# Kernel tuning notes

Hardware: AMD Instinct MI355X
Metric: run time of the kernel (lower is better)

The kernel has to match this reference:

```python
import jax, jax.numpy as jnp
import numpy as np

NUM_GRAPHS = 8
NEG_SLOPE = 0.2


def add_self_loops(edge_index, n):
    loops = jnp.arange(n, dtype=edge_index.dtype)
    src = jnp.concatenate([edge_index[0], loops])
    dst = jnp.concatenate([edge_index[1], loops])
    return src, dst


def gat_conv(x, src, dst, W, att_src, att_dst, bias, concat):
    # x: [N, F_in]; W: [F_in, H*C]; att_src/att_dst: [H, C]; bias: [H*C] or [C]
    n = x.shape[0]
    H, C = att_src.shape
    xl = (x @ W).reshape(n, H, C)                     # [N, H, C]
    a_src = jnp.einsum('nhc,hc->nh', xl, att_src)     # [N, H]
    a_dst = jnp.einsum('nhc,hc->nh', xl, att_dst)     # [N, H]
    e = jax.nn.leaky_relu(a_src[src] + a_dst[dst], NEG_SLOPE)  # [E, H]
    # segment softmax over edges grouped by destination node
    m = jax.ops.segment_max(e, dst, num_segments=n)   # [N, H]
    e = jnp.exp(e - m[dst])
    denom = jax.ops.segment_sum(e, dst, num_segments=n)
    alpha = e / (denom[dst] + 1e-16)                  # [E, H]
    msg = xl[src] * alpha[:, :, None]                 # [E, H, C]
    out = jax.ops.segment_sum(msg, dst, num_segments=n)  # [N, H, C]
    out = out.reshape(n, H * C) if concat else out.mean(axis=1)
    return out + bias


def global_mean_pool(x, batch, num_graphs):
    s = jax.ops.segment_sum(x, batch, num_segments=num_graphs)
    cnt = jax.ops.segment_sum(jnp.ones((x.shape[0],), x.dtype), batch, num_segments=num_graphs)
    return s / jnp.maximum(cnt, 1.0)[:, None]


def setup_inputs() -> dict:
    key = jax.random.key(0)
    ks = jax.random.split(key, 12)
    N, E, F_in, Ch, H, F_out = 50000, 800000, 128, 64, 4, 128
    x = jax.random.normal(ks[0], (N, F_in), dtype=jnp.float32)
    edge_index = jax.random.randint(ks[1], (2, E), 0, N, dtype=jnp.int64)
    batch = jnp.sort(jax.random.randint(ks[2], (N,), 0, NUM_GRAPHS, dtype=jnp.int64))
    s = 0.1
    W1 = jax.random.normal(ks[3], (F_in, H * Ch), dtype=jnp.float32) * s
    att_src1 = jax.random.normal(ks[4], (H, Ch), dtype=jnp.float32) * s
    att_dst1 = jax.random.normal(ks[5], (H, Ch), dtype=jnp.float32) * s
    bias1 = jnp.zeros((H * Ch,), dtype=jnp.float32)
    W2 = jax.random.normal(ks[6], (H * Ch, F_out), dtype=jnp.float32) * s
    att_src2 = jax.random.normal(ks[7], (1, F_out), dtype=jnp.float32) * s
    att_dst2 = jax.random.normal(ks[8], (1, F_out), dtype=jnp.float32) * s
    bias2 = jnp.zeros((F_out,), dtype=jnp.float32)
    return {"x": x, "edge_index": edge_index, "batch": batch,
            "W1": W1, "att_src1": att_src1, "att_dst1": att_dst1, "bias1": bias1,
            "W2": W2, "att_src2": att_src2, "att_dst2": att_dst2, "bias2": bias2}


def reference(x, edge_index, batch, W1, att_src1, att_dst1, bias1, W2, att_src2, att_dst2, bias2):
    n = x.shape[0]
    src, dst = add_self_loops(edge_index, n)
    h = gat_conv(x, src, dst, W1, att_src1, att_dst1, bias1, concat=True)
    h = jax.nn.relu(h)
    h = gat_conv(h, src, dst, W2, att_src2, att_dst2, bias2, concat=False)
    return global_mean_pool(h, batch, NUM_GRAPHS)
```

## Files before the change

kernel.cpp:

```cpp
#include <hip/hip_runtime.h>
#include <cstdint>
#include <cstddef>

#define NEG_SLOPE 0.2f
#define LOG2E 1.44269504088896f
#define NREP 64

typedef __attribute__((ext_vector_type(8))) short bf16x8;
typedef __attribute__((ext_vector_type(4))) float f32x4;
typedef __attribute__((ext_vector_type(2))) float f32x2;

__device__ __forceinline__ ushort f2b(float f) {
  unsigned u = __float_as_uint(f);
  return (ushort)((u + 0x7FFFu + ((u >> 16) & 1)) >> 16);
}
__device__ __forceinline__ float fexp2(float x) {
#if __has_builtin(__builtin_amdgcn_exp2f)
  return __builtin_amdgcn_exp2f(x);
#else
  return __exp2f(x);
#endif
}
__device__ __forceinline__ int lbound(const int* __restrict__ a, int n, int key) {
  int lo = 0, hi = n;
  while (lo < hi) { int m = (lo + hi) >> 1; if (a[m] < key) lo = m + 1; else hi = m; }
  return lo;
}

__global__ __launch_bounds__(256) void setup_k(const float* __restrict__ W1,
                                               ushort* __restrict__ Bp1,
                                               const float* __restrict__ W2,
                                               ushort* __restrict__ Bp2,
                                               int* __restrict__ hist,
                                               float* __restrict__ pp, int n) {
  int i = blockIdx.x * 256 + threadIdx.x;
  {
    int k = i >> 8, c = i & 255;
    Bp1[(((size_t)(k >> 3) * 256 + c) << 3) + (k & 7)] = f2b(W1[i]);
  }
  {
    int k = i >> 7, c = i & 127;
    Bp2[(((size_t)(k >> 3) * 128 + c) << 3) + (k & 7)] = f2b(W2[i]);
  }
  if (i < n) hist[i] = 0;
  int i2 = i + 32768;
  if (i2 < n) hist[i2] = 0;
  pp[i] = 0.f;
  pp[i + 32768] = 0.f;
}

template<int N, int K, int C, int H, bool AF32>
__device__ __forceinline__ void gemm_attn_body(const void* __restrict__ A_,
                                               const ushort* __restrict__ Bp,
                                               const float* __restrict__ att_src,
                                               const float* __restrict__ att_dst,
                                               unsigned char* __restrict__ C8,
                                               float* __restrict__ a_src,
                                               float* __restrict__ a_dst,
                                               int M, int bid) {
  constexpr int ROWS = K / 8;
  __shared__ ushort Bl[ROWS * N * 8];
  const int tid = threadIdx.x;
  #pragma unroll
  for (int it = 0; it < ROWS * N / 256; ++it) {
    int id = it * 256 + tid;
    int brow = id / N, c = id % N;
    int cs = (c + 2 * brow) & (N - 1);
    *(bf16x8*)&Bl[((size_t)brow * N + cs) * 8] = *(const bf16x8*)&Bp[(size_t)id * 8];
  }
  __syncthreads();

  const int wave = tid >> 6;
  const int lane = tid & 63;
  const int strips = M / 16;
  const int strip = bid * 4 + wave;
  if (strip >= strips) return;
  const int r = lane & 15, kg = lane >> 4;
  const int nrow = strip * 16 + r;

  bf16x8 a[K / 32];
  if constexpr (AF32) {
    const float* Af = (const float*)A_;
    #pragma unroll
    for (int k0 = 0; k0 < K / 32; ++k0) {
      float4 f0 = *(const float4*)(Af + (size_t)nrow * K + k0 * 32 + kg * 8);
      float4 f1 = *(const float4*)(Af + (size_t)nrow * K + k0 * 32 + kg * 8 + 4);
      bf16x8 t;
      t[0] = (short)f2b(f0.x); t[1] = (short)f2b(f0.y);
      t[2] = (short)f2b(f0.z); t[3] = (short)f2b(f0.w);
      t[4] = (short)f2b(f1.x); t[5] = (short)f2b(f1.y);
      t[6] = (short)f2b(f1.z); t[7] = (short)f2b(f1.w);
      a[k0] = t;
    }
  } else {
    const ushort* Ab = (const ushort*)A_;
    #pragma unroll
    for (int k0 = 0; k0 < K / 32; ++k0)
      a[k0] = *(const bf16x8*)(Ab + (size_t)nrow * K + k0 * 32 + kg * 8);
  }

  float as_p = 0.f, ad_p = 0.f;
  #pragma unroll
  for (int n0 = 0; n0 < N / 16; ++n0) {
    f32x4 acc = {0.f, 0.f, 0.f, 0.f};
    #pragma unroll
    for (int k0 = 0; k0 < K / 32; ++k0) {
      int brow = k0 * 4 + kg;
      int cs = (n0 * 16 + r + 2 * brow) & (N - 1);
      bf16x8 b = *(const bf16x8*)&Bl[((size_t)brow * N + cs) * 8];
      acc = __builtin_amdgcn_mfma_f32_16x16x32_bf16(b, a[k0], acc, 0, 0, 0);
    }
    float4 avs = *(const float4*)(att_src + n0 * 16 + kg * 4);
    float4 avd = *(const float4*)(att_dst + n0 * 16 + kg * 4);
    as_p += acc[0] * avs.x + acc[1] * avs.y + acc[2] * avs.z + acc[3] * avs.w;
    ad_p += acc[0] * avd.x + acc[1] * avd.y + acc[2] * avd.z + acc[3] * avd.w;
    int dw = __builtin_amdgcn_cvt_pk_fp8_f32(acc[0], acc[1], 0, false);
    dw = __builtin_amdgcn_cvt_pk_fp8_f32(acc[2], acc[3], dw, true);
    *(unsigned*)(C8 + (size_t)nrow * N + (uint)(n0 * 16 + kg * 4)) = (unsigned)dw;
    if (((n0 + 1) * 16) % C == 0) {
      float ts = as_p * LOG2E, td = ad_p * LOG2E;
      ts += __shfl_xor(ts, 16); ts += __shfl_xor(ts, 32);
      td += __shfl_xor(td, 16); td += __shfl_xor(td, 32);
      if (kg == 0) {
        int h = (n0 * 16) / C;
        a_src[(size_t)nrow * H + h] = ts;
        a_dst[(size_t)nrow * H + h] = td;
      }
      as_p = 0.f; ad_p = 0.f;
    }
  }
}

template<int N, int K, int C, int H, bool AF32>
__global__ __launch_bounds__(256) void gemm_rank_k(const void* __restrict__ A_,
                                                   const ushort* __restrict__ Bp,
                                                   const float* __restrict__ att_src,
                                                   const float* __restrict__ att_dst,
                                                   unsigned char* __restrict__ C8,
                                                   float* __restrict__ a_src,
                                                   float* __restrict__ a_dst, int M,
                                                   const int* __restrict__ edst,
                                                   int* __restrict__ hist,
                                                   int* __restrict__ rank,
                                                   int E, int GB) {
  if ((int)blockIdx.x < GB) {
    gemm_attn_body<N, K, C, H, AF32>(A_, Bp, att_src, att_dst, C8,
                                     a_src, a_dst, M, blockIdx.x);
  } else {
    int base = ((blockIdx.x - GB) * 256 + threadIdx.x) * 8;
    #pragma unroll
    for (int u = 0; u < 8; ++u) {
      int e = base + u;
      if (e < E) rank[e] = atomicAdd(hist + edst[e], 1);
    }
  }
}

template<int N, int K, int C, int H, bool AF32>
__global__ __launch_bounds__(256) void gemm_attn_k(const void* __restrict__ A_,
                                                   const ushort* __restrict__ Bp,
                                                   const float* __restrict__ att_src,
                                                   const float* __restrict__ att_dst,
                                                   unsigned char* __restrict__ C8,
                                                   float* __restrict__ a_src,
                                                   float* __restrict__ a_dst, int M) {
  gemm_attn_body<N, K, C, H, AF32>(A_, Bp, att_src, att_dst, C8,
                                   a_src, a_dst, M, blockIdx.x);
}

__global__ __launch_bounds__(256) void scan1_k(const int* __restrict__ hist,
                                               int* __restrict__ excl,
                                               int* __restrict__ chunksum, int n) {
  __shared__ int sums[256];
  int base = blockIdx.x * 1024 + threadIdx.x * 4;
  int4 v = {0, 0, 0, 0};
  if (base + 3 < n) v = *(const int4*)(hist + base);
  else {
    if (base < n)     v.x = hist[base];
    if (base + 1 < n) v.y = hist[base + 1];
    if (base + 2 < n) v.z = hist[base + 2];
    if (base + 3 < n) v.w = hist[base + 3];
  }
  int s = v.x + v.y + v.z + v.w;
  sums[threadIdx.x] = s;
  __syncthreads();
  for (int off = 1; off < 256; off <<= 1) {
    int t = (threadIdx.x >= (unsigned)off) ? sums[threadIdx.x - off] : 0;
    __syncthreads();
    sums[threadIdx.x] += t;
    __syncthreads();
  }
  if (threadIdx.x == 255) chunksum[blockIdx.x] = sums[255];
  int e0 = sums[threadIdx.x] - s;
  int e1 = e0 + v.x, e2 = e1 + v.y, e3 = e2 + v.z;
  if (base + 3 < n) {
    int4 o = {e0, e1, e2, e3};
    *(int4*)(excl + base) = o;
  } else {
    if (base < n)     excl[base] = e0;
    if (base + 1 < n) excl[base + 1] = e1;
    if (base + 2 < n) excl[base + 2] = e2;
    if (base + 3 < n) excl[base + 3] = e3;
  }
}

__global__ void scan2_k(const int* __restrict__ chunksum,
                        int* __restrict__ chunkoff, int nchunks) {
  if (threadIdx.x == 0) {
    int run = 0;
    for (int c = 0; c < nchunks; ++c) { chunkoff[c] = run; run += chunksum[c]; }
  }
}

__global__ __launch_bounds__(256) void addoff_k(int* __restrict__ rowptr,
                                                const int* __restrict__ chunkoff,
                                                int n, int total) {
  int i = blockIdx.x * 256 + threadIdx.x;
  if (i == 0) rowptr[n] = total;
  if (i >= n) return;
  rowptr[i] += chunkoff[i >> 10];
}

__global__ __launch_bounds__(256) void fill_k(const int* __restrict__ esrc,
                                              const int* __restrict__ edst,
                                              const int* __restrict__ rowptr,
                                              const int* __restrict__ rank,
                                              int* __restrict__ csr_src,
                                              int E, int Epad) {
  int e = blockIdx.x * 256 + threadIdx.x;
  if (e < E) csr_src[rowptr[edst[e]] + rank[e]] = esrc[e];
  else if (e < Epad) csr_src[e] = 0;
}

template<int H, int C>
__global__ __launch_bounds__(256) void agg1_k(const int* __restrict__ rowptr,
                                              const int* __restrict__ csr,
                                              const float* __restrict__ a_src,
                                              const float* __restrict__ a_dst,
                                              const unsigned char* __restrict__ xl,
                                              const float* __restrict__ bias,
                                              ushort* __restrict__ out, int n) {
  constexpr int F = H * C;
  const int wid0 = (blockIdx.x * 256 + threadIdx.x) >> 6;
  if (wid0 >= n) return;
  const int wid = __builtin_amdgcn_readfirstlane(wid0);
  const int lane = threadIdx.x & 63;
  const int h = lane >> 4;
  const uint lofs = (uint)lane * 4;
  const int j4 = lane & 3;
  const int je = lane >> 2;
  const int beg = rowptr[wid];
  const int end = rowptr[wid + 1];

  const float adh_s = a_dst[(uint)wid * 4 + j4];
  float vs_s = a_src[(uint)wid * 4 + j4] + adh_s;
  vs_s = fmaxf(vs_s, NEG_SLOPE * vs_s);

  float den = 1.f;
  float acc[4];
  {
    uint xs = *(const uint*)(xl + ((uint)wid * F + lofs));
    f32x2 lo = __builtin_amdgcn_cvt_pk_f32_fp8(xs, false);
    f32x2 hi = __builtin_amdgcn_cvt_pk_f32_fp8(xs, true);
    acc[0] = lo[0]; acc[1] = lo[1]; acc[2] = hi[0]; acc[3] = hi[1];
  }

  for (int j = beg; j < end; j += 16) {
    int sl = csr[j + je];
    float t = a_src[(uint)sl * 4 + j4] + adh_s;
    t = fmaxf(t, NEG_SLOPE * t);
    t = (j + je < end) ? t - vs_s : -1e30f;
    float pl = fexp2(t);
    uint xv[16];
    #pragma unroll
    for (int u = 0; u < 16; ++u) {
      int su = csr[j + u];
      xv[u] = *(const uint*)(xl + ((uint)su * F + lofs));
    }
    #pragma unroll
    for (int u = 0; u < 16; ++u) {
      float pu = __shfl(pl, u * 4 + h);
      den += pu;
      f32x2 lo = __builtin_amdgcn_cvt_pk_f32_fp8(xv[u], false);
      f32x2 hi = __builtin_amdgcn_cvt_pk_f32_fp8(xv[u], true);
      acc[0] = fmaf(pu, lo[0], acc[0]);
      acc[1] = fmaf(pu, lo[1], acc[1]);
      acc[2] = fmaf(pu, hi[0], acc[2]);
      acc[3] = fmaf(pu, hi[1], acc[3]);
    }
  }

  float inv = 1.f / (den + 1e-16f);
  float o[4];
  #pragma unroll
  for (int i = 0; i < 4; ++i)
    o[i] = fmaxf(fmaf(acc[i], inv, bias[lane * 4 + i]), 0.f);
  ushort4 ov = {f2b(o[0]), f2b(o[1]), f2b(o[2]), f2b(o[3])};
  *(ushort4*)(out + (size_t)wid * F + lane * 4) = ov;
}

__global__ __launch_bounds__(256) void agg2pool_k(const int* __restrict__ rowptr,
                                                  const int* __restrict__ csr,
                                                  const float* __restrict__ a_src,
                                                  const float* __restrict__ a_dst,
                                                  const unsigned char* __restrict__ xl,
                                                  const int* __restrict__ batch,
                                                  float* __restrict__ pp,
                                                  int n, int Emax) {
  const int pair = (blockIdx.x * 256 + threadIdx.x) >> 6;
  const int lane = threadIdx.x & 63;
  const int l32 = lane & 31;
  const int half = lane >> 5;
  int wid = pair * 2 + half;
  const bool act = wid < n;
  if (!act) wid = n - 1;
  const uint lofs = (uint)l32 * 4;
  const int beg = rowptr[wid];
  const int deg = rowptr[wid + 1] - beg;
  const int mdeg = max(deg, __shfl_xor(deg, 32));
  const float adh = a_dst[wid];

  float vs = a_src[wid] + adh;
  vs = fmaxf(vs, NEG_SLOPE * vs);
  float den = 1.f;
  float acc[4];
  {
    uint xs = *(const uint*)(xl + ((uint)wid * 128 + lofs));
    f32x2 lo = __builtin_amdgcn_cvt_pk_f32_fp8(xs, false);
    f32x2 hi = __builtin_amdgcn_cvt_pk_f32_fp8(xs, true);
    acc[0] = lo[0]; acc[1] = lo[1]; acc[2] = hi[0]; acc[3] = hi[1];
  }

  for (int j = 0; j < mdeg; j += 32) {
    int sl = csr[min(beg + j + l32, Emax)];
    float t = a_src[sl] + adh;
    t = fmaxf(t, NEG_SLOPE * t);
    t = (j + l32 < deg) ? t - vs : -1e30f;
    float pl = fexp2(t);
    #pragma unroll
    for (int g = 0; g < 2; ++g) {
      int su[16];
      uint xv[16];
      #pragma unroll
      for (int u = 0; u < 16; ++u) {
        su[u] = __shfl(sl, half * 32 + g * 16 + u);
        xv[u] = *(const uint*)(xl + ((uint)su[u] * 128 + lofs));
      }
      #pragma unroll
      for (int u = 0; u < 16; ++u) {
        float pu = __shfl(pl, half * 32 + g * 16 + u);
        den += pu;
        f32x2 lo = __builtin_amdgcn_cvt_pk_f32_fp8(xv[u], false);
        f32x2 hi = __builtin_amdgcn_cvt_pk_f32_fp8(xv[u], true);
        acc[0] = fmaf(pu, lo[0], acc[0]);
        acc[1] = fmaf(pu, lo[1], acc[1]);
        acc[2] = fmaf(pu, hi[0], acc[2]);
        acc[3] = fmaf(pu, hi[1], acc[3]);
      }
    }
  }

  __shared__ float red[8][128];
  __shared__ int gids[8];
  const int rrow = (threadIdx.x >> 6) * 2 + half;
  float inv = act ? 1.f / (den + 1e-16f) : 0.f;
  float4 ov = {acc[0] * inv, acc[1] * inv, acc[2] * inv, acc[3] * inv};
  *(float4*)&red[rrow][l32 * 4] = ov;
  if (l32 == 0) gids[rrow] = act ? batch[wid] : -1;
  __syncthreads();
  if (threadIdx.x < 128) {
    const int ch = threadIdx.x;
    float* base = pp + (size_t)(blockIdx.x & (NREP - 1)) * 8 * 128;
    float sum = 0.f;
    int cur = gids[0];
    #pragma unroll
    for (int r = 0; r < 8; ++r) {
      int g = gids[r];
      if (g != cur) {
        if (cur >= 0) unsafeAtomicAdd(base + cur * 128 + ch, sum);
        sum = 0.f;
        cur = g;
      }
      if (g >= 0) sum += red[r][ch];
    }
    if (cur >= 0) unsafeAtomicAdd(base + cur * 128 + ch, sum);
  }
}

__global__ __launch_bounds__(256) void finalize_k(const float* __restrict__ pp,
                                                  const int* __restrict__ batch,
                                                  const float* __restrict__ bias2,
                                                  float* __restrict__ out, int n) {
  int t = blockIdx.x * 256 + threadIdx.x;
  if (t >= 8 * 128) return;
  int g = t >> 7, c = t & 127;
  float s = 0.f;
  #pragma unroll 8
  for (int rep = 0; rep < NREP; ++rep) s += pp[rep * 8 * 128 + t];
  int lo = lbound(batch, n, g);
  int hi = lbound(batch, n, g + 1);
  float cnt = (float)(hi - lo);
  out[t] = s / fmaxf(cnt, 1.f) + bias2[c];
}

extern "C" void kernel_launch(void* const* d_in, const int* in_sizes, int n_in,
                              void* d_out, int out_size, void* d_ws, size_t ws_size,
                              hipStream_t stream) {
  const float* x        = (const float*)d_in[0];
  const int*   ei       = (const int*)d_in[1];
  const int*   batch    = (const int*)d_in[2];
  const float* W1       = (const float*)d_in[3];
  const float* att_src1 = (const float*)d_in[4];
  const float* att_dst1 = (const float*)d_in[5];
  const float* bias1    = (const float*)d_in[6];
  const float* W2       = (const float*)d_in[7];
  const float* att_src2 = (const float*)d_in[8];
  const float* att_dst2 = (const float*)d_in[9];
  const float* bias2    = (const float*)d_in[10];
  float* out = (float*)d_out;

  const int E  = in_sizes[1] / 2;
  const int NN = in_sizes[2];
  const int* esrc = ei;
  const int* edst = ei + E;
  const int PAD = 64;

  char* w = (char*)d_ws;
  size_t woff = 0;
  auto walloc = [&](size_t bytes) -> char* {
    char* r = w + woff;
    woff += (bytes + 255) & ~(size_t)255;
    return r;
  };
  unsigned char* xl1 = (unsigned char*)walloc((size_t)NN * 256);
  ushort* h1     = (ushort*)walloc((size_t)NN * 256 * 2);
  unsigned char* xl2 = (unsigned char*)walloc((size_t)NN * 128);
  float*  a_src1 = (float*)walloc((size_t)NN * 4 * 4);
  float*  a_dst1 = (float*)walloc((size_t)NN * 4 * 4);
  float*  a_src2 = (float*)walloc((size_t)NN * 4);
  float*  a_dst2 = (float*)walloc((size_t)NN * 4);
  int*    rowptr = (int*)walloc((size_t)(NN + 1) * 4);
  int*    hist   = (int*)walloc((size_t)NN * 4);
  int*    rank   = (int*)walloc((size_t)E * 4);
  int*    csrsrc = (int*)walloc((size_t)(E + PAD) * 4);
  ushort* Bp1    = (ushort*)walloc(128 * 256 * 2);
  ushort* Bp2    = (ushort*)walloc(256 * 128 * 2);
  int*    chunks = (int*)walloc(256 * 4);
  int*    chunko = (int*)walloc(256 * 4);
  float*  pp     = (float*)walloc((size_t)NREP * 8 * 128 * 4);

  dim3 blk(256);
  const int nbEp = (E + PAD + 255) / 256;
  const int nbN4 = (NN + 3) / 4;
  const int nbP  = ((NN + 1) / 2 + 3) / 4;
  const int strips = NN / 16;
  const int gblocks = (strips + 3) / 4;
  const int rankBlocks = (E + 2047) / 2048;
  const int nchunks = (NN + 1023) / 1024;

  setup_k<<<128, blk, 0, stream>>>(W1, Bp1, W2, Bp2, hist, pp, NN);

  gemm_rank_k<256, 128, 64, 4, true><<<gblocks + rankBlocks, blk, 0, stream>>>(
      x, Bp1, att_src1, att_dst1, xl1, a_src1, a_dst1, NN,
      edst, hist, rank, E, gblocks);

  scan1_k<<<nchunks, blk, 0, stream>>>(hist, rowptr, chunks, NN);
  scan2_k<<<1, 64, 0, stream>>>(chunks, chunko, nchunks);
  addoff_k<<<(NN + 255) / 256, blk, 0, stream>>>(rowptr, chunko, NN, E);

  fill_k<<<nbEp, blk, 0, stream>>>(esrc, edst, rowptr, rank, csrsrc, E, E + PAD);

  agg1_k<4, 64><<<nbN4, blk, 0, stream>>>(
      rowptr, csrsrc, a_src1, a_dst1, xl1, bias1, h1, NN);

  gemm_attn_k<128, 256, 128, 1, false><<<gblocks, blk, 0, stream>>>(
      h1, Bp2, att_src2, att_dst2, xl2, a_src2, a_dst2, NN);

  agg2pool_k<<<nbP, blk, 0, stream>>>(
      rowptr, csrsrc, a_src2, a_dst2, xl2, batch, pp, NN, E + PAD - 1);

  finalize_k<<<4, blk, 0, stream>>>(pp, batch, bias2, out, NN);
}
```

Baseline: 164.4 us.

## Split rank and GEMM kernels, read B weights from global instead of LDS

Separates the fused GEMM+edge-rank kernel into a standalone rank kernel and a plain GEMM kernel. The GEMM no longer stages the packed bf16 weight matrix into swizzled shared memory and instead loads B fragments straight from global memory (L2-cached), with the n0 loop unroll reduced to 2. This removes the per-block LDS fill and barrier and lowers LDS use for occupancy. In exchange, every MFMA operand now comes from global memory, the rank atomics no longer overlap with the GEMM, and there is one extra kernel launch.

```diff
diff --git a/kernel.cpp b/kernel.cpp
--- a/kernel.cpp
+++ b/kernel.cpp
@@ -49,31 +49,29 @@
   pp[i + 32768] = 0.f;
 }
 
+__global__ __launch_bounds__(256) void rank_k(const int* __restrict__ edst,
+                                              int* __restrict__ hist,
+                                              int* __restrict__ rank, int E) {
+  int base = (blockIdx.x * 256 + threadIdx.x) * 8;
+  #pragma unroll
+  for (int u = 0; u < 8; ++u) {
+    int e = base + u;
+    if (e < E) rank[e] = atomicAdd(hist + edst[e], 1);
+  }
+}
+
 template<int N, int K, int C, int H, bool AF32>
-__device__ __forceinline__ void gemm_attn_body(const void* __restrict__ A_,
-                                               const ushort* __restrict__ Bp,
-                                               const float* __restrict__ att_src,
-                                               const float* __restrict__ att_dst,
-                                               unsigned char* __restrict__ C8,
-                                               float* __restrict__ a_src,
-                                               float* __restrict__ a_dst,
-                                               int M, int bid) {
-  constexpr int ROWS = K / 8;
-  __shared__ ushort Bl[ROWS * N * 8];
-  const int tid = threadIdx.x;
-  #pragma unroll
-  for (int it = 0; it < ROWS * N / 256; ++it) {
-    int id = it * 256 + tid;
-    int brow = id / N, c = id % N;
-    int cs = (c + 2 * brow) & (N - 1);
-    *(bf16x8*)&Bl[((size_t)brow * N + cs) * 8] = *(const bf16x8*)&Bp[(size_t)id * 8];
-  }
-  __syncthreads();
-
-  const int wave = tid >> 6;
-  const int lane = tid & 63;
+__global__ __launch_bounds__(256) void gemm_attn_k(const void* __restrict__ A_,
+                                                   const ushort* __restrict__ Bp,
+                                                   const float* __restrict__ att_src,
+                                                   const float* __restrict__ att_dst,
+                                                   unsigned char* __restrict__ C8,
+                                                   float* __restrict__ a_src,
+                                                   float* __restrict__ a_dst, int M) {
+  const int wave = threadIdx.x >> 6;
+  const int lane = threadIdx.x & 63;
   const int strips = M / 16;
-  const int strip = bid * 4 + wave;
+  const int strip = blockIdx.x * 4 + wave;
   if (strip >= strips) return;
   const int r = lane & 15, kg = lane >> 4;
   const int nrow = strip * 16 + r;
@@ -100,14 +98,12 @@
   }
 
   float as_p = 0.f, ad_p = 0.f;
-  #pragma unroll
+  #pragma unroll 2
   for (int n0 = 0; n0 < N / 16; ++n0) {
     f32x4 acc = {0.f, 0.f, 0.f, 0.f};
     #pragma unroll
     for (int k0 = 0; k0 < K / 32; ++k0) {
-      int brow = k0 * 4 + kg;
-      int cs = (n0 * 16 + r + 2 * brow) & (N - 1);
-      bf16x8 b = *(const bf16x8*)&Bl[((size_t)brow * N + cs) * 8];
+      bf16x8 b = *(const bf16x8*)(Bp + ((size_t)(k0 * 4 + kg) * N + n0 * 16 + r) * 8);
       acc = __builtin_amdgcn_mfma_f32_16x16x32_bf16(b, a[k0], acc, 0, 0, 0);
     }
     float4 avs = *(const float4*)(att_src + n0 * 16 + kg * 4);
@@ -129,43 +125,6 @@
       as_p = 0.f; ad_p = 0.f;
     }
   }
-}
-
-template<int N, int K, int C, int H, bool AF32>
-__global__ __launch_bounds__(256) void gemm_rank_k(const void* __restrict__ A_,
-                                                   const ushort* __restrict__ Bp,
-                                                   const float* __restrict__ att_src,
-                                                   const float* __restrict__ att_dst,
-                                                   unsigned char* __restrict__ C8,
-                                                   float* __restrict__ a_src,
-                                                   float* __restrict__ a_dst, int M,
-                                                   const int* __restrict__ edst,
-                                                   int* __restrict__ hist,
-                                                   int* __restrict__ rank,
-                                                   int E, int GB) {
-  if ((int)blockIdx.x < GB) {
-    gemm_attn_body<N, K, C, H, AF32>(A_, Bp, att_src, att_dst, C8,
-                                     a_src, a_dst, M, blockIdx.x);
-  } else {
-    int base = ((blockIdx.x - GB) * 256 + threadIdx.x) * 8;
-    #pragma unroll
-    for (int u = 0; u < 8; ++u) {
-      int e = base + u;
-      if (e < E) rank[e] = atomicAdd(hist + edst[e], 1);
-    }
-  }
-}
-
-template<int N, int K, int C, int H, bool AF32>
-__global__ __launch_bounds__(256) void gemm_attn_k(const void* __restrict__ A_,
-                                                   const ushort* __restrict__ Bp,
-                                                   const float* __restrict__ att_src,
-                                                   const float* __restrict__ att_dst,
-                                                   unsigned char* __restrict__ C8,
-                                                   float* __restrict__ a_src,
-                                                   float* __restrict__ a_dst, int M) {
-  gemm_attn_body<N, K, C, H, AF32>(A_, Bp, att_src, att_dst, C8,
-                                   a_src, a_dst, M, blockIdx.x);
 }
 
 __global__ __launch_bounds__(256) void scan1_k(const int* __restrict__ hist,
@@ -460,9 +419,10 @@
 
   setup_k<<<128, blk, 0, stream>>>(W1, Bp1, W2, Bp2, hist, pp, NN);
 
-  gemm_rank_k<256, 128, 64, 4, true><<<gblocks + rankBlocks, blk, 0, stream>>>(
-      x, Bp1, att_src1, att_dst1, xl1, a_src1, a_dst1, NN,
-      edst, hist, rank, E, gblocks);
+  rank_k<<<rankBlocks, blk, 0, stream>>>(edst, hist, rank, E);
+
+  gemm_attn_k<256, 128, 64, 4, true><<<gblocks, blk, 0, stream>>>(
+      x, Bp1, att_src1, att_dst1, xl1, a_src1, a_dst1, NN);
 
   scan1_k<<<nchunks, blk, 0, stream>>>(hist, rowptr, chunks, NN);
   scan2_k<<<1, 64, 0, stream>>>(chunks, chunko, nchunks);
```

After: 184.5 us. 12.3% more time.

## Split edge histogram into four replicas and read GEMM weights directly from global

Applied to the files above, without the earlier changes.

The destination-degree histogram is split into four sub-histograms indexed by edge id mod 4, which spreads atomic contention across replicas. The scan kernel now builds per-replica prefix offsets, and the CSR fill adds those offsets to compute each edge's slot. Separately, the GEMM no longer stages the packed weight matrix into LDS with a barrier; it loads B fragments straight from global/L2, and the n-loop unroll is reduced to 2. This removes the LDS staging and sync but adds more global loads per MFMA and extra memory traffic in the scan and fill kernels.

```diff
diff --git a/kernel.cpp b/kernel.cpp
--- a/kernel.cpp
+++ b/kernel.cpp
@@ -31,8 +31,8 @@
                                                ushort* __restrict__ Bp1,
                                                const float* __restrict__ W2,
                                                ushort* __restrict__ Bp2,
-                                               int* __restrict__ hist,
-                                               float* __restrict__ pp, int n) {
+                                               int* __restrict__ hist, int ns4,
+                                               float* __restrict__ pp) {
   int i = blockIdx.x * 256 + threadIdx.x;
   {
     int k = i >> 8, c = i & 255;
@@ -42,9 +42,7 @@
     int k = i >> 7, c = i & 127;
     Bp2[(((size_t)(k >> 3) * 128 + c) << 3) + (k & 7)] = f2b(W2[i]);
   }
-  if (i < n) hist[i] = 0;
-  int i2 = i + 32768;
-  if (i2 < n) hist[i2] = 0;
+  for (int j = i; j < ns4; j += 32768) hist[j] = 0;
   pp[i] = 0.f;
   pp[i + 32768] = 0.f;
 }
@@ -58,20 +56,8 @@
                                                float* __restrict__ a_src,
                                                float* __restrict__ a_dst,
                                                int M, int bid) {
-  constexpr int ROWS = K / 8;
-  __shared__ ushort Bl[ROWS * N * 8];
-  const int tid = threadIdx.x;
-  #pragma unroll
-  for (int it = 0; it < ROWS * N / 256; ++it) {
-    int id = it * 256 + tid;
-    int brow = id / N, c = id % N;
-    int cs = (c + 2 * brow) & (N - 1);
-    *(bf16x8*)&Bl[((size_t)brow * N + cs) * 8] = *(const bf16x8*)&Bp[(size_t)id * 8];
-  }
-  __syncthreads();
-
-  const int wave = tid >> 6;
-  const int lane = tid & 63;
+  const int wave = threadIdx.x >> 6;
+  const int lane = threadIdx.x & 63;
   const int strips = M / 16;
   const int strip = bid * 4 + wave;
   if (strip >= strips) return;
@@ -100,14 +86,12 @@
   }
 
   float as_p = 0.f, ad_p = 0.f;
-  #pragma unroll
+  #pragma unroll 2
   for (int n0 = 0; n0 < N / 16; ++n0) {
     f32x4 acc = {0.f, 0.f, 0.f, 0.f};
     #pragma unroll
     for (int k0 = 0; k0 < K / 32; ++k0) {
-      int brow = k0 * 4 + kg;
-      int cs = (n0 * 16 + r + 2 * brow) & (N - 1);
-      bf16x8 b = *(const bf16x8*)&Bl[((size_t)brow * N + cs) * 8];
+      bf16x8 b = *(const bf16x8*)(Bp + ((size_t)(k0 * 4 + kg) * N + n0 * 16 + r) * 8);
       acc = __builtin_amdgcn_mfma_f32_16x16x32_bf16(b, a[k0], acc, 0, 0, 0);
     }
     float4 avs = *(const float4*)(att_src + n0 * 16 + kg * 4);
@@ -140,7 +124,7 @@
                                                    float* __restrict__ a_src,
                                                    float* __restrict__ a_dst, int M,
                                                    const int* __restrict__ edst,
-                                                   int* __restrict__ hist,
+                                                   int* __restrict__ hist, int ns,
                                                    int* __restrict__ rank,
                                                    int E, int GB) {
   if ((int)blockIdx.x < GB) {
@@ -151,7 +135,8 @@
     #pragma unroll
     for (int u = 0; u < 8; ++u) {
       int e = base + u;
-      if (e < E) rank[e] = atomicAdd(hist + edst[e], 1);
+      if (e < E)
+        rank[e] = atomicAdd(hist + (e & 3) * ns + edst[e], 1);
     }
   }
 }
@@ -168,31 +153,47 @@
                                    a_src, a_dst, M, blockIdx.x);
 }
 
-__global__ __launch_bounds__(256) void scan1_k(const int* __restrict__ hist,
-                                               int* __restrict__ excl,
-                                               int* __restrict__ chunksum, int n) {
+__global__ __launch_bounds__(256) void scan1r_k(const int* __restrict__ hist, int ns,
+                                                int* __restrict__ roff,
+                                                int* __restrict__ excl,
+                                                int* __restrict__ chunksum, int n) {
   __shared__ int sums[256];
   int base = blockIdx.x * 1024 + threadIdx.x * 4;
-  int4 v = {0, 0, 0, 0};
-  if (base + 3 < n) v = *(const int4*)(hist + base);
-  else {
-    if (base < n)     v.x = hist[base];
-    if (base + 1 < n) v.y = hist[base + 1];
-    if (base + 2 < n) v.z = hist[base + 2];
-    if (base + 3 < n) v.w = hist[base + 3];
-  }
-  int s = v.x + v.y + v.z + v.w;
+  int4 t = {0, 0, 0, 0};
+  if (base + 3 < n) {
+    int4 c0 = *(const int4*)(hist + base);
+    int4 c1 = *(const int4*)(hist + ns + base);
+    int4 c2 = *(const int4*)(hist + 2 * ns + base);
+    int4 c3 = *(const int4*)(hist + 3 * ns + base);
+    int4 r1 = c0;
+    int4 r2 = {r1.x + c1.x, r1.y + c1.y, r1.z + c1.z, r1.w + c1.w};
+    int4 r3 = {r2.x + c2.x, r2.y + c2.y, r2.z + c2.z, r2.w + c2.w};
+    *(int4*)(roff + base) = r1;
+    *(int4*)(roff + ns + base) = r2;
+    *(int4*)(roff + 2 * ns + base) = r3;
+    t.x = r3.x + c3.x; t.y = r3.y + c3.y; t.z = r3.z + c3.z; t.w = r3.w + c3.w;
+  } else {
+    for (int q = 0; q < 4; ++q) {
+      int i = base + q;
+      if (i < n) {
+        int c0 = hist[i], c1 = hist[ns + i], c2 = hist[2 * ns + i], c3 = hist[3 * ns + i];
+        roff[i] = c0; roff[ns + i] = c0 + c1; roff[2 * ns + i] = c0 + c1 + c2;
+        ((int*)&t)[q] = c0 + c1 + c2 + c3;
+      }
+    }
+  }
+  int s = t.x + t.y + t.z + t.w;
   sums[threadIdx.x] = s;
   __syncthreads();
   for (int off = 1; off < 256; off <<= 1) {
-    int t = (threadIdx.x >= (unsigned)off) ? sums[threadIdx.x - off] : 0;
+    int v = (threadIdx.x >= (unsigned)off) ? sums[threadIdx.x - off] : 0;
     __syncthreads();
-    sums[threadIdx.x] += t;
+    sums[threadIdx.x] += v;
     __syncthreads();
   }
   if (threadIdx.x == 255) chunksum[blockIdx.x] = sums[255];
   int e0 = sums[threadIdx.x] - s;
-  int e1 = e0 + v.x, e2 = e1 + v.y, e3 = e2 + v.z;
+  int e1 = e0 + t.x, e2 = e1 + t.y, e3 = e2 + t.z;
   if (base + 3 < n) {
     int4 o = {e0, e1, e2, e3};
     *(int4*)(excl + base) = o;
@@ -224,12 +225,19 @@
 __global__ __launch_bounds__(256) void fill_k(const int* __restrict__ esrc,
                                               const int* __restrict__ edst,
                                               const int* __restrict__ rowptr,
+                                              const int* __restrict__ roff, int ns,
                                               const int* __restrict__ rank,
                                               int* __restrict__ csr_src,
                                               int E, int Epad) {
   int e = blockIdx.x * 256 + threadIdx.x;
-  if (e < E) csr_src[rowptr[edst[e]] + rank[e]] = esrc[e];
-  else if (e < Epad) csr_src[e] = 0;
+  if (e < E) {
+    int d = edst[e];
+    int r = e & 3;
+    int ro = (r == 0) ? 0 : roff[(r - 1) * ns + d];
+    csr_src[rowptr[d] + ro + rank[e]] = esrc[e];
+  } else if (e < Epad) {
+    csr_src[e] = 0;
+  }
 }
 
 template<int H, int C>
@@ -424,6 +432,7 @@
   const int* esrc = ei;
   const int* edst = ei + E;
   const int PAD = 64;
+  const int ns = (NN + 3) & ~3;
 
   char* w = (char*)d_ws;
   size_t woff = 0;
@@ -440,7 +449,8 @@
   float*  a_src2 = (float*)walloc((size_t)NN * 4);
   float*  a_dst2 = (float*)walloc((size_t)NN * 4);
   int*    rowptr = (int*)walloc((size_t)(NN + 1) * 4);
-  int*    hist   = (int*)walloc((size_t)NN * 4);
+  int*    hist   = (int*)walloc((size_t)ns * 4 * 4);
+  int*    roff   = (int*)walloc((size_t)ns * 3 * 4);
   int*    rank   = (int*)walloc((size_t)E * 4);
   int*    csrsrc = (int*)walloc((size_t)(E + PAD) * 4);
   ushort* Bp1    = (ushort*)walloc(128 * 256 * 2);
@@ -458,17 +468,18 @@
   const int rankBlocks = (E + 2047) / 2048;
   const int nchunks = (NN + 1023) / 1024;
 
-  setup_k<<<128, blk, 0, stream>>>(W1, Bp1, W2, Bp2, hist, pp, NN);
+  setup_k<<<128, blk, 0, stream>>>(W1, Bp1, W2, Bp2, hist, ns * 4, pp);
 
   gemm_rank_k<256, 128, 64, 4, true><<<gblocks + rankBlocks, blk, 0, stream>>>(
       x, Bp1, att_src1, att_dst1, xl1, a_src1, a_dst1, NN,
-      edst, hist, rank, E, gblocks);
-
-  scan1_k<<<nchunks, blk, 0, stream>>>(hist, rowptr, chunks, NN);
+      edst, hist, ns, rank, E, gblocks);
+
+  scan1r_k<<<nchunks, blk, 0, stream>>>(hist, ns, roff, rowptr, chunks, NN);
   scan2_k<<<1, 64, 0, stream>>>(chunks, chunko, nchunks);
   addoff_k<<<(NN + 255) / 256, blk, 0, stream>>>(rowptr, chunko, NN, E);
 
-  fill_k<<<nbEp, blk, 0, stream>>>(esrc, edst, rowptr, rank, csrsrc, E, E + PAD);
+  fill_k<<<nbEp, blk, 0, stream>>>(esrc, edst, rowptr, roff, ns, rank,
+                                   csrsrc, E, E + PAD);
 
   agg1_k<4, 64><<<nbN4, blk, 0, stream>>>(
       rowptr, csrsrc, a_src1, a_dst1, xl1, bias1, h1, NN);
```

After: 166.3 us. About the same (+1.2%).

## Fold scan2 into scan1 via last-block atomic and read GEMM B from global

Applied to the files above, without the earlier changes.

The single-block chunk-offset scan kernel is removed. The last scan1 block to finish, detected with an atomic counter that setup_k resets, now computes the chunk offsets, which saves a kernel launch. Separately, the GEMM no longer stages the packed B matrix in LDS with a barrier and reads it straight from global memory, relying on cache, with the n-loop unroll reduced to 2. Dropping the LDS stage removes the per-block copy and sync, but B reads now go through the cache hierarchy instead of LDS, which may cost latency inside the MFMA loop.

```diff
diff --git a/kernel.cpp b/kernel.cpp
--- a/kernel.cpp
+++ b/kernel.cpp
@@ -31,9 +31,11 @@
                                                ushort* __restrict__ Bp1,
                                                const float* __restrict__ W2,
                                                ushort* __restrict__ Bp2,
-                                               int* __restrict__ hist,
-                                               float* __restrict__ pp, int n) {
+                                               int* __restrict__ hist, int ns,
+                                               float* __restrict__ pp,
+                                               int* __restrict__ done) {
   int i = blockIdx.x * 256 + threadIdx.x;
+  if (i == 0) *done = 0;
   {
     int k = i >> 8, c = i & 255;
     Bp1[(((size_t)(k >> 3) * 256 + c) << 3) + (k & 7)] = f2b(W1[i]);
@@ -42,9 +44,7 @@
     int k = i >> 7, c = i & 127;
     Bp2[(((size_t)(k >> 3) * 128 + c) << 3) + (k & 7)] = f2b(W2[i]);
   }
-  if (i < n) hist[i] = 0;
-  int i2 = i + 32768;
-  if (i2 < n) hist[i2] = 0;
+  for (int j = i; j < ns; j += 32768) hist[j] = 0;
   pp[i] = 0.f;
   pp[i + 32768] = 0.f;
 }
@@ -58,20 +58,8 @@
                                                float* __restrict__ a_src,
                                                float* __restrict__ a_dst,
                                                int M, int bid) {
-  constexpr int ROWS = K / 8;
-  __shared__ ushort Bl[ROWS * N * 8];
-  const int tid = threadIdx.x;
-  #pragma unroll
-  for (int it = 0; it < ROWS * N / 256; ++it) {
-    int id = it * 256 + tid;
-    int brow = id / N, c = id % N;
-    int cs = (c + 2 * brow) & (N - 1);
-    *(bf16x8*)&Bl[((size_t)brow * N + cs) * 8] = *(const bf16x8*)&Bp[(size_t)id * 8];
-  }
-  __syncthreads();
-
-  const int wave = tid >> 6;
-  const int lane = tid & 63;
+  const int wave = threadIdx.x >> 6;
+  const int lane = threadIdx.x & 63;
   const int strips = M / 16;
   const int strip = bid * 4 + wave;
   if (strip >= strips) return;
@@ -100,14 +88,12 @@
   }
 
   float as_p = 0.f, ad_p = 0.f;
-  #pragma unroll
+  #pragma unroll 2
   for (int n0 = 0; n0 < N / 16; ++n0) {
     f32x4 acc = {0.f, 0.f, 0.f, 0.f};
     #pragma unroll
     for (int k0 = 0; k0 < K / 32; ++k0) {
-      int brow = k0 * 4 + kg;
-      int cs = (n0 * 16 + r + 2 * brow) & (N - 1);
-      bf16x8 b = *(const bf16x8*)&Bl[((size_t)brow * N + cs) * 8];
+      bf16x8 b = *(const bf16x8*)(Bp + ((size_t)(k0 * 4 + kg) * N + n0 * 16 + r) * 8);
       acc = __builtin_amdgcn_mfma_f32_16x16x32_bf16(b, a[k0], acc, 0, 0, 0);
     }
     float4 avs = *(const float4*)(att_src + n0 * 16 + kg * 4);
@@ -170,7 +156,9 @@
 
 __global__ __launch_bounds__(256) void scan1_k(const int* __restrict__ hist,
                                                int* __restrict__ excl,
-                                               int* __restrict__ chunksum, int n) {
+                                               int* __restrict__ chunksum,
+                                               int* __restrict__ chunkoff,
+                                               int* __restrict__ done, int n) {
   __shared__ int sums[256];
   int base = blockIdx.x * 1024 + threadIdx.x * 4;
   int4 v = {0, 0, 0, 0};
@@ -190,7 +178,10 @@
     sums[threadIdx.x] += t;
     __syncthreads();
   }
-  if (threadIdx.x == 255) chunksum[blockIdx.x] = sums[255];
+  if (threadIdx.x == 255) {
+    chunksum[blockIdx.x] = sums[255];
+    __threadfence();
+  }
   int e0 = sums[threadIdx.x] - s;
   int e1 = e0 + v.x, e2 = e1 + v.y, e3 = e2 + v.z;
   if (base + 3 < n) {
@@ -202,13 +193,14 @@
     if (base + 2 < n) excl[base + 2] = e2;
     if (base + 3 < n) excl[base + 3] = e3;
   }
-}
-
-__global__ void scan2_k(const int* __restrict__ chunksum,
-                        int* __restrict__ chunkoff, int nchunks) {
+  __syncthreads();
   if (threadIdx.x == 0) {
-    int run = 0;
-    for (int c = 0; c < nchunks; ++c) { chunkoff[c] = run; run += chunksum[c]; }
+    int old = atomicAdd(done, 1);
+    if (old == (int)gridDim.x - 1) {
+      __threadfence();
+      int run = 0;
+      for (int c = 0; c < (int)gridDim.x; ++c) { chunkoff[c] = run; run += chunksum[c]; }
+    }
   }
 }
 
@@ -447,6 +439,7 @@
   ushort* Bp2    = (ushort*)walloc(256 * 128 * 2);
   int*    chunks = (int*)walloc(256 * 4);
   int*    chunko = (int*)walloc(256 * 4);
+  int*    done   = (int*)walloc(256);
   float*  pp     = (float*)walloc((size_t)NREP * 8 * 128 * 4);
 
   dim3 blk(256);
@@ -458,14 +451,13 @@
   const int rankBlocks = (E + 2047) / 2048;
   const int nchunks = (NN + 1023) / 1024;
 
-  setup_k<<<128, blk, 0, stream>>>(W1, Bp1, W2, Bp2, hist, pp, NN);
+  setup_k<<<128, blk, 0, stream>>>(W1, Bp1, W2, Bp2, hist, NN, pp, done);
 
   gemm_rank_k<256, 128, 64, 4, true><<<gblocks + rankBlocks, blk, 0, stream>>>(
       x, Bp1, att_src1, att_dst1, xl1, a_src1, a_dst1, NN,
       edst, hist, rank, E, gblocks);
 
-  scan1_k<<<nchunks, blk, 0, stream>>>(hist, rowptr, chunks, NN);
-  scan2_k<<<1, 64, 0, stream>>>(chunks, chunko, nchunks);
+  scan1_k<<<nchunks, blk, 0, stream>>>(hist, rowptr, chunks, chunko, done, NN);
   addoff_k<<<(NN + 255) / 256, blk, 0, stream>>>(rowptr, chunko, NN, E);
 
   fill_k<<<nbEp, blk, 0, stream>>>(esrc, edst, rowptr, rank, csrsrc, E, E + PAD);
```

Measured after the change: 168.0 us. 2.2% more time.
